# Kernel optimization log

Measured on AMD Instinct MI355X. Metric: run time of the kernel, lower is better.

## Reference

```python
import jax, jax.numpy as jnp
import numpy as np

V, E, H, T = 100000, 128, 256, 7
B, S = 64, 512
START, STOP = 5, 6
H2 = H // 2


def setup_inputs() -> dict:
    key = jax.random.key(0)
    ks = jax.random.split(key, 16)
    rn = lambda k, shape, s=0.1: jax.random.normal(k, shape, jnp.float32) * s
    inp = {}
    inp["sentence"] = jax.random.randint(ks[0], (B, S), 0, V)
    inp["tags"] = jax.random.randint(ks[1], (B, S), 0, 5)
    inp["h0"] = jax.random.normal(ks[2], (2, B, H2), jnp.float32)
    inp["c0"] = jax.random.normal(ks[3], (2, B, H2), jnp.float32)
    inp["embedding"] = rn(ks[4], (V, E), 1.0)
    inp["w_ih_f"] = rn(ks[5], (4 * H2, E)); inp["w_hh_f"] = rn(ks[6], (4 * H2, H2))
    inp["b_ih_f"] = rn(ks[7], (4 * H2,)); inp["b_hh_f"] = rn(ks[8], (4 * H2,))
    inp["w_ih_b"] = rn(ks[9], (4 * H2, E)); inp["w_hh_b"] = rn(ks[10], (4 * H2, H2))
    inp["b_ih_b"] = rn(ks[11], (4 * H2,)); inp["b_hh_b"] = rn(ks[12], (4 * H2,))
    inp["w_out"] = rn(ks[13], (T, H)); inp["b_out"] = rn(ks[14], (T,))
    trans = jax.random.normal(ks[15], (T, T), jnp.float32)
    trans = trans.at[START, :].set(-10000.0).at[:, STOP].set(-10000.0)
    inp["transitions"] = trans
    return inp


def _lstm_dir(x, h0, c0, wih, whh, bih, bhh, reverse):
    # x: [S, B, E]; PyTorch gate order i, f, g, o
    def step(carry, xt):
        h, c = carry
        z = xt @ wih.T + h @ whh.T + bih + bhh  # [B, 4*H2]
        i, f, g, o = jnp.split(z, 4, axis=-1)
        c = jax.nn.sigmoid(f) * c + jax.nn.sigmoid(i) * jnp.tanh(g)
        h = jax.nn.sigmoid(o) * jnp.tanh(c)
        return (h, c), h
    _, hs = jax.lax.scan(step, (h0, c0), x, reverse=reverse)
    return hs  # [S, B, H2]


def reference(sentence, tags, h0, c0, embedding, w_ih_f, w_hh_f, b_ih_f, b_hh_f,
              w_ih_b, w_hh_b, b_ih_b, b_hh_b, w_out, b_out, transitions):
    # Embedding; torch code does .view(S, B, -1) on a [B, S, E] tensor (raw
    # reinterpretation) -- replicate with reshape to match the math exactly.
    embeds = embedding[sentence].reshape(S, B, E)
    hf = _lstm_dir(embeds, h0[0], c0[0], w_ih_f, w_hh_f, b_ih_f, b_hh_f, False)
    hb = _lstm_dir(embeds, h0[1], c0[1], w_ih_b, w_hh_b, b_ih_b, b_hh_b, True)
    feats = jnp.concatenate([hf, hb], axis=-1) @ w_out.T + b_out  # [S, B, T]

    # CRF forward algorithm. Original uses transitions.t(), i.e. step score
    # for prev=i -> next=j is transitions[i, j].
    alpha0 = jnp.full((B, T), -10000.0, jnp.float32).at[:, START].set(0.0)
    def crf_step(alpha, feat):
        # [b, i, j]: alpha[b,i] + transitions[i,j]; LSE over i, add emit[b,j]
        a = jax.nn.logsumexp(alpha[:, :, None] + transitions[None, :, :], axis=1) + feat
        return a, None
    alpha, _ = jax.lax.scan(crf_step, alpha0, feats)
    fwd_score = jax.nn.logsumexp(alpha + transitions[STOP][None, :], axis=1)  # [B]

    # Gold path score: transitions[next, prev] + emit[next], per _score_sentence.
    tags_ext = jnp.concatenate([jnp.full((B, 1), START, tags.dtype), tags], axis=1)
    t_prev, t_next = tags_ext[:, :-1], tags_ext[:, 1:]  # [B, S]
    trans_sc = transitions[t_next, t_prev].sum(axis=1)
    emit_sc = jnp.take_along_axis(jnp.transpose(feats, (1, 0, 2)),
                                  t_next[:, :, None], axis=2)[..., 0].sum(axis=1)
    gold = trans_sc + emit_sc + transitions[STOP, tags_ext[:, -1]]
    return jnp.sum(fwd_score - gold) / B
```

## Files before the change

kernel.cpp:

```cpp
#include <hip/hip_runtime.h>

typedef unsigned int u32;
typedef unsigned short u16;
typedef __attribute__((ext_vector_type(8))) short short8;
typedef __attribute__((ext_vector_type(4))) float f32x4;

#define DEV __device__ __forceinline__
#define LOG2E 1.44269504089f

DEV u16 f2bf(float f) {
    u32 u = __float_as_uint(f);
    return (u16)((u + 0x7FFFu + ((u >> 16) & 1u)) >> 16);
}
DEV float bf2f(u16 h) { return __uint_as_float(((u32)h) << 16); }
DEV float frcp(float x) { return __builtin_amdgcn_rcpf(x); }
DEV float fexp2(float x) {
#if __has_builtin(__builtin_amdgcn_exp2f)
    return __builtin_amdgcn_exp2f(x);
#else
    return exp2f(x);
#endif
}
DEV u32 pack_bf16(float a, float b) {
#if __has_builtin(__builtin_amdgcn_cvt_pk_bf16_f32)
    auto v = __builtin_amdgcn_cvt_pk_bf16_f32(a, b);
    u32 r; __builtin_memcpy(&r, &v, 4); return r;
#else
    return (u32)f2bf(a) | ((u32)f2bf(b) << 16);
#endif
}
DEV float xex(uint2 v, int r) {
    u32 u = (r & 2) ? v.y : v.x;
    return (r & 1) ? __uint_as_float(u & 0xFFFF0000u) : __uint_as_float(u << 16);
}

__global__ __launch_bounds__(512) void k_inproj2(
    const int* __restrict__ sent, const float* __restrict__ emb,
    const float* __restrict__ wihf, const float* __restrict__ bihf, const float* __restrict__ bhhf,
    const float* __restrict__ wihb, const float* __restrict__ bihb, const float* __restrict__ bhhb,
    u16* __restrict__ Xf, u16* __restrict__ Xb)
{
    int blk = blockIdx.x;
    int d  = blk >> 7;
    int sc = blk & 127;
    const float* wih = d ? wihb : wihf;
    const float* bih = d ? bihb : bihf;
    const float* bhh = d ? bhhb : bhhf;
    u16* X = d ? Xb : Xf;
    int tid = threadIdx.x;
    int w = tid >> 6, lane = tid & 63;
    int rg = lane >> 4, cn = lane & 15;

    short8 afr[4][4];
    #pragma unroll
    for (int mi = 0; mi < 4; ++mi) {
        int gate = 16 * (w + 8 * mi) + cn;
        #pragma unroll
        for (int kt = 0; kt < 4; ++kt) {
            const float* p = wih + (size_t)gate * 128 + kt * 32 + rg * 8;
            float4 f0 = *(const float4*)p;
            float4 f1 = *(const float4*)(p + 4);
            union { short8 v; u32 u[4]; } sv;
            sv.u[0] = pack_bf16(f0.x, f0.y);
            sv.u[1] = pack_bf16(f0.z, f0.w);
            sv.u[2] = pack_bf16(f1.x, f1.y);
            sv.u[3] = pack_bf16(f1.z, f1.w);
            afr[mi][kt] = sv.v;
        }
    }
    float bs[4][4];
    #pragma unroll
    for (int mi = 0; mi < 4; ++mi)
        #pragma unroll
        for (int r = 0; r < 4; ++r) {
            int g = 16 * (w + 8 * mi) + 4 * rg + r;
            bs[mi][r] = bih[g] + bhh[g];
        }

    __shared__ u16 tile[2][64][136];
    #pragma unroll
    for (int stage = 0; stage < 2; ++stage) {
        if (stage) __syncthreads();
        {
            int row = tid >> 2, q = tid & 3;
            int sl = row >> 6, bb = row & 63;
            int tok = sent[(sc * 4 + stage * 2 + sl) * 64 + bb];
            const float* er = emb + (size_t)tok * 128 + q * 32;
            u16* dst = &tile[sl][bb][q * 32];
            #pragma unroll
            for (int u = 0; u < 4; ++u) {
                float4 a = *(const float4*)(er + u * 8);
                float4 c = *(const float4*)(er + u * 8 + 4);
                uint4 st;
                st.x = pack_bf16(a.x, a.y); st.y = pack_bf16(a.z, a.w);
                st.z = pack_bf16(c.x, c.y); st.w = pack_bf16(c.z, c.w);
                *(uint4*)(dst + u * 8) = st;
            }
        }
        __syncthreads();
        #pragma unroll
        for (int ss = 0; ss < 2; ++ss) {
            int s = sc * 4 + stage * 2 + ss;
            #pragma unroll
            for (int nt = 0; nt < 4; ++nt) {
                short8 bfr[4];
                #pragma unroll
                for (int kt = 0; kt < 4; ++kt)
                    bfr[kt] = *(const short8*)&tile[ss][nt * 16 + cn][kt * 32 + rg * 8];
                #pragma unroll
                for (int mi = 0; mi < 4; ++mi) {
                    f32x4 acc = {0.f, 0.f, 0.f, 0.f};
                    #pragma unroll
                    for (int kt = 0; kt < 4; ++kt)
                        acc = __builtin_amdgcn_mfma_f32_16x16x32_bf16(afr[mi][kt], bfr[kt], acc, 0, 0, 0);
                    size_t base = (((size_t)s * 4 + nt) * 32 + (w + 8 * mi)) * 256
                                + (size_t)rg * 64 + (size_t)cn * 4;
                    uint2 st;
                    st.x = pack_bf16((acc[0] + bs[mi][0]) * LOG2E, (acc[1] + bs[mi][1]) * LOG2E);
                    st.y = pack_bf16((acc[2] + bs[mi][2]) * LOG2E, (acc[3] + bs[mi][3]) * LOG2E);
                    *(uint2*)(X + base) = st;
                }
            }
        }
    }
}

__global__ __launch_bounds__(512) void k_lstm(
    const float* __restrict__ h0, const float* __restrict__ c0,
    const float* __restrict__ whhf, const float* __restrict__ whhb,
    const u16* __restrict__ Xf, const u16* __restrict__ Xb,
    u16* __restrict__ hfo, u16* __restrict__ hbo)
{
    int d  = blockIdx.x >> 2, g4 = blockIdx.x & 3;
    const float* whh = d ? whhb : whhf;
    const u16*   X   = d ? Xb   : Xf;
    u16*         ho  = d ? hbo  : hfo;
    int w = threadIdx.x >> 6, lane = threadIdx.x & 63;
    int rg = lane >> 4, cn = lane & 15;

    short8 afr[4][4];
    #pragma unroll
    for (int mi = 0; mi < 4; ++mi) {
        int gate = 16 * (w + 8 * mi) + cn;
        #pragma unroll
        for (int kt = 0; kt < 4; ++kt) {
            const float* p = whh + (size_t)gate * 128 + kt * 32 + rg * 8;
            float4 f0 = *(const float4*)p;
            float4 f1 = *(const float4*)(p + 4);
            union { short8 v; u32 u[4]; } sv;
            sv.u[0] = pack_bf16(f0.x * LOG2E, f0.y * LOG2E);
            sv.u[1] = pack_bf16(f0.z * LOG2E, f0.w * LOG2E);
            sv.u[2] = pack_bf16(f1.x * LOG2E, f1.y * LOG2E);
            sv.u[3] = pack_bf16(f1.z * LOG2E, f1.w * LOG2E);
            afr[mi][kt] = sv.v;
        }
    }
    int b = g4 * 16 + cn;
    int chb = 16 * w + rg * 4;
    float cst[4];
    {
        float4 cv = *(const float4*)(c0 + ((size_t)d * 64 + b) * 128 + chb);
        cst[0]=cv.x; cst[1]=cv.y; cst[2]=cv.z; cst[3]=cv.w;
    }
    __shared__ u16 hbuf[2][16][136];
    {
        float4 hv = *(const float4*)(h0 + ((size_t)d * 64 + b) * 128 + chb);
        uint2 st0;
        st0.x = pack_bf16(hv.x, hv.y);
        st0.y = pack_bf16(hv.z, hv.w);
        *(uint2*)&hbuf[0][cn][chb] = st0;
    }
    __syncthreads();

    int s0 = d ? 511 : 0;
    const int sdB = d ? -65536 : 65536;
    const int hdB = d ? -16384 : 16384;

    int voffB[4];
    #pragma unroll
    for (int mi = 0; mi < 4; ++mi)
        voffB[mi] = 2 * ((w + 8 * mi) * 256 + rg * 64 + cn * 4);
    const char* xbase = (const char*)X + ((size_t)s0 * 32768 + (size_t)g4 * 8192) * 2;
    uint2 xA[4], xB[4];
    #pragma unroll
    for (int mi = 0; mi < 4; ++mi) {
        xA[mi] = *(const uint2*)(xbase + voffB[mi]);
        xB[mi] = *(const uint2*)(xbase + sdB + voffB[mi]);
    }
    const char* sxA = xbase + 2 * sdB;
    const char* sxB = xbase + 3 * sdB;
    int vhoff = 2 * (b * 128 + chb);
    char* hsp = (char*)ho + (size_t)s0 * 16384;

#define LSTM_STEP(RB, WB, XC, SX)                                            \
    do {                                                                     \
        short8 bfr[4];                                                       \
        _Pragma("unroll")                                                    \
        for (int kt = 0; kt < 4; ++kt)                                       \
            bfr[kt] = *(const short8*)&hbuf[RB][cn][kt * 32 + rg * 8];       \
        f32x4 z[4];                                                          \
        _Pragma("unroll")                                                    \
        for (int mi = 0; mi < 4; ++mi) {                                     \
            f32x4 acc;                                                       \
            acc[0] = xex(XC[mi], 0); acc[1] = xex(XC[mi], 1);                \
            acc[2] = xex(XC[mi], 2); acc[3] = xex(XC[mi], 3);                \
            _Pragma("unroll")                                                \
            for (int kt = 0; kt < 4; ++kt)                                   \
                acc = __builtin_amdgcn_mfma_f32_16x16x32_bf16(               \
                    afr[mi][kt], bfr[kt], acc, 0, 0, 0);                     \
            z[mi] = acc;                                                     \
            XC[mi] = *(const uint2*)(SX + voffB[mi]);                        \
        }                                                                    \
        SX += 2 * sdB;                                                       \
        float hnew[4];                                                       \
        _Pragma("unroll")                                                    \
        for (int r = 0; r < 4; ++r) {                                        \
            float zi = z[0][r], zf = z[1][r], zg = z[2][r], zo = z[3][r];    \
            float ei = fexp2(-zi);                                           \
            float ef = fexp2(-zf);                                           \
            float eo = fexp2(-zo);                                           \
            float eg = fexp2(fminf(zg + zg, 126.f));                         \
            float A = 1.f + ei, F = 1.f + ef, G = 1.f + eg, O = 1.f + eo;    \
            float AG = A * G;                                                \
            float num = fmaf(cst[r], AG, (eg - 1.f) * F);                    \
            float cc  = num * frcp(F * AG);                                  \
            cst[r] = cc;                                                     \
            float ec = fexp2(fminf(2.885390082f * cc, 126.f));               \
            hnew[r] = (ec - 1.f) * frcp(fmaf(O, ec, O));                     \
        }                                                                    \
        uint2 st;                                                            \
        st.x = pack_bf16(hnew[0], hnew[1]);                                  \
        st.y = pack_bf16(hnew[2], hnew[3]);                                  \
        *(uint2*)&hbuf[WB][cn][chb] = st;                                    \
        *(uint2*)(hsp + vhoff) = st;                                         \
        hsp += hdB;                                                          \
        asm volatile("s_waitcnt lgkmcnt(0)\n\ts_barrier" ::: "memory");      \
    } while (0)

    for (int it = 0; it < 256; ++it) {
        LSTM_STEP(0, 1, xA, sxA);
        LSTM_STEP(1, 0, xB, sxB);
    }
#undef LSTM_STEP
}

__global__ __launch_bounds__(256) void k_feats(
    const u16* __restrict__ hf, const u16* __restrict__ hb,
    const float* __restrict__ wout, const float* __restrict__ bout,
    float* __restrict__ feats)
{
    __shared__ u16 sf[32][136], sb[32][136];
    __shared__ float wo[7][260];
    __shared__ float bo[8];
    int tid = threadIdx.x;
    int pos0 = blockIdx.x * 32;
    {
        int r = tid >> 3, cc = (tid & 7) * 16;
        const uint4* pf = (const uint4*)(hf + (size_t)(pos0 + r) * 128 + cc);
        const uint4* pb = (const uint4*)(hb + (size_t)(pos0 + r) * 128 + cc);
        *(uint4*)&sf[r][cc]     = pf[0];
        *(uint4*)&sf[r][cc + 8] = pf[1];
        *(uint4*)&sb[r][cc]     = pb[0];
        *(uint4*)&sb[r][cc + 8] = pb[1];
    }
    for (int i = tid; i < 1792; i += 256) wo[i >> 8][i & 255] = wout[i];
    if (tid < 7) bo[tid] = bout[tid];
    __syncthreads();
    int pp = tid >> 3, tt = tid & 7;
    if (tt < 7) {
        float acc = bo[tt];
        #pragma unroll 4
        for (int ch = 0; ch < 128; ++ch)
            acc += bf2f(sf[pp][ch]) * wo[tt][ch]
                 + bf2f(sb[pp][ch]) * wo[tt][128 + ch];
        feats[(size_t)(pos0 + pp) * 7 + tt] = acc;
    }
}

__global__ __launch_bounds__(64) void k_crf_chunk(
    const float* __restrict__ feats, const float* __restrict__ trans,
    float* __restrict__ chunkM)
{
    int b = blockIdx.x >> 3, c = blockIdx.x & 7;
    int lane = threadIdx.x;
    int i = lane >> 3, j = lane & 7;
    __shared__ float M[8][8];
    __shared__ float fl[64][8];
    int s0 = c * 64;
    for (int idx = lane; idx < 448; idx += 64) {
        int ss = idx / 7, jj = idx - ss * 7;
        fl[ss][jj] = feats[(size_t)((s0 + ss) * 64 + b) * 7 + jj];
    }
    float tc[7];
    #pragma unroll
    for (int k = 0; k < 7; ++k) tc[k] = (j < 7) ? trans[k * 7 + j] : 0.f;
    __syncthreads();
    M[i][j] = (i < 7 && j < 7) ? (trans[i * 7 + j] + fl[0][j]) : -1e30f;
    __syncthreads();
    for (int ss = 1; ss < 64; ++ss) {
        float4 m0 = *(const float4*)&M[i][0];
        float4 m1 = *(const float4*)&M[i][4];
        float v0 = m0.x + tc[0], v1 = m0.y + tc[1], v2 = m0.z + tc[2];
        float v3 = m0.w + tc[3], v4 = m1.x + tc[4], v5 = m1.y + tc[5];
        float v6 = m1.z + tc[6];
        float mx = fmaxf(fmaxf(fmaxf(v0, v1), fmaxf(v2, v3)),
                         fmaxf(fmaxf(v4, v5), v6));
        float sm = __expf(v0 - mx) + __expf(v1 - mx) + __expf(v2 - mx)
                 + __expf(v3 - mx) + __expf(v4 - mx) + __expf(v5 - mx)
                 + __expf(v6 - mx);
        float r = mx + __logf(sm) + fl[ss][j];
        __syncthreads();
        if (i < 7 && j < 7) M[i][j] = r;
        __syncthreads();
    }
    if (i < 7 && j < 7)
        chunkM[(size_t)(b * 8 + c) * 49 + i * 7 + j] = M[i][j];
}

__global__ __launch_bounds__(64) void k_crf_final(
    const float* __restrict__ chunkM, const float* __restrict__ trans,
    const int* __restrict__ tags, const float* __restrict__ feats,
    float* __restrict__ out)
{
    int b = blockIdx.x;
    int lane = threadIdx.x;
    __shared__ float P[8][49];
    __shared__ float Tl[49];
    __shared__ float av[2][8];
    __shared__ int   tg[512];
    for (int idx = lane; idx < 392; idx += 64)
        P[idx / 49][idx % 49] = chunkM[(size_t)b * 392 + idx];
    if (lane < 49) Tl[lane] = trans[lane];
    for (int idx = lane; idx < 512; idx += 64) tg[idx] = tags[(size_t)b * 512 + idx];
    if (lane < 8) av[0][lane] = (lane == 5) ? 0.f : -1e4f;
    __syncthreads();
    int cur = 0;
    for (int cch = 0; cch < 8; ++cch) {
        if (lane < 7) {
            float vv[7], mx = -1e30f;
            #pragma unroll
            for (int ii = 0; ii < 7; ++ii) {
                vv[ii] = av[cur][ii] + P[cch][ii * 7 + lane];
                mx = fmaxf(mx, vv[ii]);
            }
            float sm = 0.f;
            #pragma unroll
            for (int ii = 0; ii < 7; ++ii) sm += __expf(vv[ii] - mx);
            av[cur ^ 1][lane] = mx + __logf(sm);
        }
        __syncthreads();
        cur ^= 1;
    }
    float mx = -1e30f, uu[7];
    #pragma unroll
    for (int jj = 0; jj < 7; ++jj) {
        uu[jj] = av[cur][jj] + Tl[6 * 7 + jj];
        mx = fmaxf(mx, uu[jj]);
    }
    float sm = 0.f;
    #pragma unroll
    for (int jj = 0; jj < 7; ++jj) sm += __expf(uu[jj] - mx);
    float fwd = mx + __logf(sm);
    float acc = 0.f;
    for (int ss = lane; ss < 512; ss += 64) {
        int tn = tg[ss];
        int tp = (ss == 0) ? 5 : tg[ss - 1];
        acc += Tl[tn * 7 + tp] + feats[(size_t)(ss * 64 + b) * 7 + tn];
    }
    #pragma unroll
    for (int mk = 32; mk >= 1; mk >>= 1) acc += __shfl_xor(acc, mk, 64);
    if (lane == 0) {
        float gold = acc + Tl[6 * 7 + tg[511]];
        atomicAdd(out, (fwd - gold) * (1.0f / 64.0f));
    }
}

extern "C" void kernel_launch(void* const* d_in, const int* in_sizes, int n_in,
                              void* d_out, int out_size, void* d_ws, size_t ws_size,
                              hipStream_t stream) {
    const int*   sent = (const int*)d_in[0];
    const int*   tags = (const int*)d_in[1];
    const float* h0   = (const float*)d_in[2];
    const float* c0   = (const float*)d_in[3];
    const float* emb  = (const float*)d_in[4];
    const float* wihf = (const float*)d_in[5];
    const float* whhf = (const float*)d_in[6];
    const float* bihf = (const float*)d_in[7];
    const float* bhhf = (const float*)d_in[8];
    const float* wihb = (const float*)d_in[9];
    const float* whhb = (const float*)d_in[10];
    const float* bihb = (const float*)d_in[11];
    const float* bhhb = (const float*)d_in[12];
    const float* wout = (const float*)d_in[13];
    const float* bout = (const float*)d_in[14];
    const float* trn  = (const float*)d_in[15];

    char* ws = (char*)d_ws;
    u16*   Xf     = (u16*)(ws);
    u16*   Xb     = (u16*)(ws + 33554432);
    u16*   hfp    = (u16*)(ws + 67108864);
    u16*   hbp    = (u16*)(ws + 75497472);
    float* feats  = (float*)(ws + 83886080);
    float* chunkM = (float*)(ws + 84803584);

    hipMemsetAsync(d_out, 0, 4, stream);
    k_inproj2<<<256, 512, 0, stream>>>(sent, emb, wihf, bihf, bhhf,
                                       wihb, bihb, bhhb, Xf, Xb);
    k_lstm<<<8, 512, 0, stream>>>(h0, c0, whhf, whhb, Xf, Xb, hfp, hbp);
    k_feats<<<1024, 256, 0, stream>>>(hfp, hbp, wout, bout, feats);
    k_crf_chunk<<<512, 64, 0, stream>>>(feats, trn, chunkM);
    k_crf_final<<<64, 64, 0, stream>>>(chunkM, trn, tags, feats, (float*)d_out);
}
```

Baseline: 576.3 us.

## Fuse input projection into recurrent LSTM kernel with prefetched embedding ring

Removes the separate input-projection kernel and its 64MB bf16 intermediate. The LSTM kernel now computes the W_ih·x term each step with extra MFMAs, using embedding rows prefetched a few steps ahead into a shared ring buffer. Hidden outputs are staged in an 8-slot shared ring and written to global memory in coalesced batches every 8 steps. This doubles the MFMA work on the serial critical path in exchange for dropping global traffic and a kernel launch, and it adds an extra barrier every 8 steps.

Result: slower. 694.3 us (+20.5%).

```diff
diff --git a/kernel.cpp b/kernel.cpp
--- a/kernel.cpp
+++ b/kernel.cpp
@@ -29,192 +29,131 @@
     return (u32)f2bf(a) | ((u32)f2bf(b) << 16);
 #endif
 }
-DEV float xex(uint2 v, int r) {
-    u32 u = (r & 2) ? v.y : v.x;
-    return (r & 1) ? __uint_as_float(u & 0xFFFF0000u) : __uint_as_float(u << 16);
-}
-
-__global__ __launch_bounds__(512) void k_inproj2(
+
+__global__ __launch_bounds__(512) void k_lstm(
     const int* __restrict__ sent, const float* __restrict__ emb,
-    const float* __restrict__ wihf, const float* __restrict__ bihf, const float* __restrict__ bhhf,
-    const float* __restrict__ wihb, const float* __restrict__ bihb, const float* __restrict__ bhhb,
-    u16* __restrict__ Xf, u16* __restrict__ Xb)
+    const float* __restrict__ h0, const float* __restrict__ c0,
+    const float* __restrict__ whhf, const float* __restrict__ whhb,
+    const float* __restrict__ wihf, const float* __restrict__ wihb,
+    const float* __restrict__ bihf, const float* __restrict__ bhhf,
+    const float* __restrict__ bihb, const float* __restrict__ bhhb,
+    u16* __restrict__ hfo, u16* __restrict__ hbo)
 {
-    int blk = blockIdx.x;
-    int d  = blk >> 7;
-    int sc = blk & 127;
+    const int d  = blockIdx.x >> 2, g4 = blockIdx.x & 3;
+    const float* whh = d ? whhb : whhf;
     const float* wih = d ? wihb : wihf;
     const float* bih = d ? bihb : bihf;
     const float* bhh = d ? bhhb : bhhf;
-    u16* X = d ? Xb : Xf;
-    int tid = threadIdx.x;
-    int w = tid >> 6, lane = tid & 63;
-    int rg = lane >> 4, cn = lane & 15;
-
-    short8 afr[4][4];
+    u16* ho = d ? hbo : hfo;
+    const int tid = threadIdx.x;
+    const int w = tid >> 6, lane = tid & 63;
+    const int rg = lane >> 4, cn = lane & 15;
+    const int row16 = tid >> 5, col32 = tid & 31;
+    const int chb = 16 * w + rg * 4;
+    const int b = g4 * 16 + cn;
+
+    __shared__ int stoks[512 * 17];
+    __shared__ __align__(16) u16 ebuf[4][16][136];
+    __shared__ __align__(16) u16 hring[8][16][136];
+
+    short8 ah[4][4], ae[4][4];
     #pragma unroll
     for (int mi = 0; mi < 4; ++mi) {
         int gate = 16 * (w + 8 * mi) + cn;
         #pragma unroll
         for (int kt = 0; kt < 4; ++kt) {
-            const float* p = wih + (size_t)gate * 128 + kt * 32 + rg * 8;
-            float4 f0 = *(const float4*)p;
-            float4 f1 = *(const float4*)(p + 4);
-            union { short8 v; u32 u[4]; } sv;
-            sv.u[0] = pack_bf16(f0.x, f0.y);
-            sv.u[1] = pack_bf16(f0.z, f0.w);
-            sv.u[2] = pack_bf16(f1.x, f1.y);
-            sv.u[3] = pack_bf16(f1.z, f1.w);
-            afr[mi][kt] = sv.v;
+            const float* ph = whh + (size_t)gate * 128 + kt * 32 + rg * 8;
+            const float* pe = wih + (size_t)gate * 128 + kt * 32 + rg * 8;
+            float4 h0v = *(const float4*)ph, h1v = *(const float4*)(ph + 4);
+            float4 e0v = *(const float4*)pe, e1v = *(const float4*)(pe + 4);
+            union { short8 v; u32 u[4]; } sh, se;
+            sh.u[0] = pack_bf16(h0v.x * LOG2E, h0v.y * LOG2E);
+            sh.u[1] = pack_bf16(h0v.z * LOG2E, h0v.w * LOG2E);
+            sh.u[2] = pack_bf16(h1v.x * LOG2E, h1v.y * LOG2E);
+            sh.u[3] = pack_bf16(h1v.z * LOG2E, h1v.w * LOG2E);
+            se.u[0] = pack_bf16(e0v.x * LOG2E, e0v.y * LOG2E);
+            se.u[1] = pack_bf16(e0v.z * LOG2E, e0v.w * LOG2E);
+            se.u[2] = pack_bf16(e1v.x * LOG2E, e1v.y * LOG2E);
+            se.u[3] = pack_bf16(e1v.z * LOG2E, e1v.w * LOG2E);
+            ah[mi][kt] = sh.v;
+            ae[mi][kt] = se.v;
         }
     }
-    float bs[4][4];
+    f32x4 bs4[4];
     #pragma unroll
     for (int mi = 0; mi < 4; ++mi)
         #pragma unroll
         for (int r = 0; r < 4; ++r) {
             int g = 16 * (w + 8 * mi) + 4 * rg + r;
-            bs[mi][r] = bih[g] + bhh[g];
+            bs4[mi][r] = (bih[g] + bhh[g]) * LOG2E;
         }
-
-    __shared__ u16 tile[2][64][136];
-    #pragma unroll
-    for (int stage = 0; stage < 2; ++stage) {
-        if (stage) __syncthreads();
-        {
-            int row = tid >> 2, q = tid & 3;
-            int sl = row >> 6, bb = row & 63;
-            int tok = sent[(sc * 4 + stage * 2 + sl) * 64 + bb];
-            const float* er = emb + (size_t)tok * 128 + q * 32;
-            u16* dst = &tile[sl][bb][q * 32];
-            #pragma unroll
-            for (int u = 0; u < 4; ++u) {
-                float4 a = *(const float4*)(er + u * 8);
-                float4 c = *(const float4*)(er + u * 8 + 4);
-                uint4 st;
-                st.x = pack_bf16(a.x, a.y); st.y = pack_bf16(a.z, a.w);
-                st.z = pack_bf16(c.x, c.y); st.w = pack_bf16(c.z, c.w);
-                *(uint4*)(dst + u * 8) = st;
-            }
-        }
-        __syncthreads();
-        #pragma unroll
-        for (int ss = 0; ss < 2; ++ss) {
-            int s = sc * 4 + stage * 2 + ss;
-            #pragma unroll
-            for (int nt = 0; nt < 4; ++nt) {
-                short8 bfr[4];
-                #pragma unroll
-                for (int kt = 0; kt < 4; ++kt)
-                    bfr[kt] = *(const short8*)&tile[ss][nt * 16 + cn][kt * 32 + rg * 8];
-                #pragma unroll
-                for (int mi = 0; mi < 4; ++mi) {
-                    f32x4 acc = {0.f, 0.f, 0.f, 0.f};
-                    #pragma unroll
-                    for (int kt = 0; kt < 4; ++kt)
-                        acc = __builtin_amdgcn_mfma_f32_16x16x32_bf16(afr[mi][kt], bfr[kt], acc, 0, 0, 0);
-                    size_t base = (((size_t)s * 4 + nt) * 32 + (w + 8 * mi)) * 256
-                                + (size_t)rg * 64 + (size_t)cn * 4;
-                    uint2 st;
-                    st.x = pack_bf16((acc[0] + bs[mi][0]) * LOG2E, (acc[1] + bs[mi][1]) * LOG2E);
-                    st.y = pack_bf16((acc[2] + bs[mi][2]) * LOG2E, (acc[3] + bs[mi][3]) * LOG2E);
-                    *(uint2*)(X + base) = st;
-                }
-            }
-        }
-    }
-}
-
-__global__ __launch_bounds__(512) void k_lstm(
-    const float* __restrict__ h0, const float* __restrict__ c0,
-    const float* __restrict__ whhf, const float* __restrict__ whhb,
-    const u16* __restrict__ Xf, const u16* __restrict__ Xb,
-    u16* __restrict__ hfo, u16* __restrict__ hbo)
-{
-    int d  = blockIdx.x >> 2, g4 = blockIdx.x & 3;
-    const float* whh = d ? whhb : whhf;
-    const u16*   X   = d ? Xb   : Xf;
-    u16*         ho  = d ? hbo  : hfo;
-    int w = threadIdx.x >> 6, lane = threadIdx.x & 63;
-    int rg = lane >> 4, cn = lane & 15;
-
-    short8 afr[4][4];
-    #pragma unroll
-    for (int mi = 0; mi < 4; ++mi) {
-        int gate = 16 * (w + 8 * mi) + cn;
-        #pragma unroll
-        for (int kt = 0; kt < 4; ++kt) {
-            const float* p = whh + (size_t)gate * 128 + kt * 32 + rg * 8;
-            float4 f0 = *(const float4*)p;
-            float4 f1 = *(const float4*)(p + 4);
-            union { short8 v; u32 u[4]; } sv;
-            sv.u[0] = pack_bf16(f0.x * LOG2E, f0.y * LOG2E);
-            sv.u[1] = pack_bf16(f0.z * LOG2E, f0.w * LOG2E);
-            sv.u[2] = pack_bf16(f1.x * LOG2E, f1.y * LOG2E);
-            sv.u[3] = pack_bf16(f1.z * LOG2E, f1.w * LOG2E);
-            afr[mi][kt] = sv.v;
-        }
-    }
-    int b = g4 * 16 + cn;
-    int chb = 16 * w + rg * 4;
     float cst[4];
     {
         float4 cv = *(const float4*)(c0 + ((size_t)d * 64 + b) * 128 + chb);
         cst[0]=cv.x; cst[1]=cv.y; cst[2]=cv.z; cst[3]=cv.w;
     }
-    __shared__ u16 hbuf[2][16][136];
+    {
+        int s = tid;
+        const int4* sp = (const int4*)(sent + s * 64 + g4 * 16);
+        int4 t0 = sp[0], t1 = sp[1], t2 = sp[2], t3 = sp[3];
+        int* dst = &stoks[s * 17];
+        dst[0]=t0.x; dst[1]=t0.y; dst[2]=t0.z; dst[3]=t0.w;
+        dst[4]=t1.x; dst[5]=t1.y; dst[6]=t1.z; dst[7]=t1.w;
+        dst[8]=t2.x; dst[9]=t2.y; dst[10]=t2.z; dst[11]=t2.w;
+        dst[12]=t3.x; dst[13]=t3.y; dst[14]=t3.z; dst[15]=t3.w;
+    }
     {
         float4 hv = *(const float4*)(h0 + ((size_t)d * 64 + b) * 128 + chb);
         uint2 st0;
         st0.x = pack_bf16(hv.x, hv.y);
         st0.y = pack_bf16(hv.z, hv.w);
-        *(uint2*)&hbuf[0][cn][chb] = st0;
-    }
-    __syncthreads();
-
-    int s0 = d ? 511 : 0;
-    const int sdB = d ? -65536 : 65536;
-    const int hdB = d ? -16384 : 16384;
-
-    int voffB[4];
-    #pragma unroll
-    for (int mi = 0; mi < 4; ++mi)
-        voffB[mi] = 2 * ((w + 8 * mi) * 256 + rg * 64 + cn * 4);
-    const char* xbase = (const char*)X + ((size_t)s0 * 32768 + (size_t)g4 * 8192) * 2;
-    uint2 xA[4], xB[4];
-    #pragma unroll
-    for (int mi = 0; mi < 4; ++mi) {
-        xA[mi] = *(const uint2*)(xbase + voffB[mi]);
-        xB[mi] = *(const uint2*)(xbase + sdB + voffB[mi]);
-    }
-    const char* sxA = xbase + 2 * sdB;
-    const char* sxB = xbase + 3 * sdB;
-    int vhoff = 2 * (b * 128 + chb);
-    char* hsp = (char*)ho + (size_t)s0 * 16384;
-
-#define LSTM_STEP(RB, WB, XC, SX)                                            \
-    do {                                                                     \
-        short8 bfr[4];                                                       \
-        _Pragma("unroll")                                                    \
-        for (int kt = 0; kt < 4; ++kt)                                       \
-            bfr[kt] = *(const short8*)&hbuf[RB][cn][kt * 32 + rg * 8];       \
+        *(uint2*)&hring[7][cn][chb] = st0;
+    }
+    #pragma unroll
+    for (int k = 0; k < 2; ++k) {
+        int s = d ? (511 - k) : k;
+        int tok = sent[s * 64 + g4 * 16 + row16];
+        float4 ev = *(const float4*)(emb + (size_t)tok * 128 + col32 * 4);
+        uint2 wv; wv.x = pack_bf16(ev.x, ev.y); wv.y = pack_bf16(ev.z, ev.w);
+        *(uint2*)&ebuf[k][row16][col32 * 4] = wv;
+    }
+    float4 pA, pB;
+    { int s = d ? 509 : 2; int tok = sent[s*64 + g4*16 + row16];
+      pA = *(const float4*)(emb + (size_t)tok * 128 + col32 * 4); }
+    { int s = d ? 508 : 3; int tok = sent[s*64 + g4*16 + row16];
+      pB = *(const float4*)(emb + (size_t)tok * 128 + col32 * 4); }
+    __syncthreads();
+
+#define SUB(U, PEND)                                                         \
+    {                                                                        \
+        const int t = it * 8 + U;                                            \
+        short8 hb[4], eb[4];                                                 \
+        _Pragma("unroll") for (int kt = 0; kt < 4; ++kt) {                   \
+            hb[kt] = *(const short8*)&hring[(U + 7) & 7][cn][kt*32 + rg*8];  \
+            eb[kt] = *(const short8*)&ebuf[U & 3][cn][kt*32 + rg*8];         \
+        }                                                                    \
         f32x4 z[4];                                                          \
-        _Pragma("unroll")                                                    \
-        for (int mi = 0; mi < 4; ++mi) {                                     \
-            f32x4 acc;                                                       \
-            acc[0] = xex(XC[mi], 0); acc[1] = xex(XC[mi], 1);                \
-            acc[2] = xex(XC[mi], 2); acc[3] = xex(XC[mi], 3);                \
-            _Pragma("unroll")                                                \
-            for (int kt = 0; kt < 4; ++kt)                                   \
+        _Pragma("unroll") for (int mi = 0; mi < 4; ++mi) {                   \
+            f32x4 acc = bs4[mi];                                             \
+            _Pragma("unroll") for (int kt = 0; kt < 4; ++kt)                 \
                 acc = __builtin_amdgcn_mfma_f32_16x16x32_bf16(               \
-                    afr[mi][kt], bfr[kt], acc, 0, 0, 0);                     \
+                    ah[mi][kt], hb[kt], acc, 0, 0, 0);                       \
+            _Pragma("unroll") for (int kt = 0; kt < 4; ++kt)                 \
+                acc = __builtin_amdgcn_mfma_f32_16x16x32_bf16(               \
+                    ae[mi][kt], eb[kt], acc, 0, 0, 0);                       \
             z[mi] = acc;                                                     \
-            XC[mi] = *(const uint2*)(SX + voffB[mi]);                        \
         }                                                                    \
-        SX += 2 * sdB;                                                       \
+        {                                                                    \
+            uint2 wv; wv.x = pack_bf16(PEND.x, PEND.y);                      \
+            wv.y = pack_bf16(PEND.z, PEND.w);                                \
+            *(uint2*)&ebuf[(U + 2) & 3][row16][col32 * 4] = wv;              \
+            int s_ = d ? (511 - (t + 4)) : (t + 4);                          \
+            s_ = s_ < 0 ? 0 : (s_ > 511 ? 511 : s_);                         \
+            int tok = stoks[s_ * 17 + row16];                                \
+            PEND = *(const float4*)(emb + (size_t)tok * 128 + col32 * 4);    \
+        }                                                                    \
         float hnew[4];                                                       \
-        _Pragma("unroll")                                                    \
-        for (int r = 0; r < 4; ++r) {                                        \
+        _Pragma("unroll") for (int r = 0; r < 4; ++r) {                      \
             float zi = z[0][r], zf = z[1][r], zg = z[2][r], zo = z[3][r];    \
             float ei = fexp2(-zi);                                           \
             float ef = fexp2(-zf);                                           \
@@ -228,20 +167,27 @@
             float ec = fexp2(fminf(2.885390082f * cc, 126.f));               \
             hnew[r] = (ec - 1.f) * frcp(fmaf(O, ec, O));                     \
         }                                                                    \
-        uint2 st;                                                            \
-        st.x = pack_bf16(hnew[0], hnew[1]);                                  \
-        st.y = pack_bf16(hnew[2], hnew[3]);                                  \
-        *(uint2*)&hbuf[WB][cn][chb] = st;                                    \
-        *(uint2*)(hsp + vhoff) = st;                                         \
-        hsp += hdB;                                                          \
+        uint2 st2;                                                           \
+        st2.x = pack_bf16(hnew[0], hnew[1]);                                 \
+        st2.y = pack_bf16(hnew[2], hnew[3]);                                 \
+        *(uint2*)&hring[U & 7][cn][chb] = st2;                               \
         asm volatile("s_waitcnt lgkmcnt(0)\n\ts_barrier" ::: "memory");      \
-    } while (0)
-
-    for (int it = 0; it < 256; ++it) {
-        LSTM_STEP(0, 1, xA, sxA);
-        LSTM_STEP(1, 0, xB, sxB);
-    }
-#undef LSTM_STEP
+    }
+
+    for (int it = 0; it < 64; ++it) {
+        SUB(0, pA); SUB(1, pB); SUB(2, pA); SUB(3, pB);
+        SUB(4, pA); SUB(5, pB); SUB(6, pA); SUB(7, pB);
+        #pragma unroll
+        for (int c = 0; c < 4; ++c) {
+            int chunk = c * 512 + tid;
+            int slot = chunk >> 8, rw = (chunk >> 4) & 15, part = chunk & 15;
+            uint4 v = *(const uint4*)&hring[slot][rw][part * 8];
+            int s_ = d ? (511 - (it * 8 + slot)) : (it * 8 + slot);
+            *(uint4*)(ho + ((size_t)s_ * 64 + g4 * 16 + rw) * 128 + part * 8) = v;
+        }
+        asm volatile("s_waitcnt lgkmcnt(0)\n\ts_barrier" ::: "memory");
+    }
+#undef SUB
 }
 
 __global__ __launch_bounds__(256) void k_feats(
@@ -396,17 +342,14 @@
     const float* trn  = (const float*)d_in[15];
 
     char* ws = (char*)d_ws;
-    u16*   Xf     = (u16*)(ws);
-    u16*   Xb     = (u16*)(ws + 33554432);
-    u16*   hfp    = (u16*)(ws + 67108864);
-    u16*   hbp    = (u16*)(ws + 75497472);
-    float* feats  = (float*)(ws + 83886080);
-    float* chunkM = (float*)(ws + 84803584);
+    u16*   hfp    = (u16*)(ws);
+    u16*   hbp    = (u16*)(ws + 8388608);
+    float* feats  = (float*)(ws + 16777216);
+    float* chunkM = (float*)(ws + 17694720);
 
     hipMemsetAsync(d_out, 0, 4, stream);
-    k_inproj2<<<256, 512, 0, stream>>>(sent, emb, wihf, bihf, bhhf,
-                                       wihb, bihb, bhhb, Xf, Xb);
-    k_lstm<<<8, 512, 0, stream>>>(h0, c0, whhf, whhb, Xf, Xb, hfp, hbp);
+    k_lstm<<<8, 512, 0, stream>>>(sent, emb, h0, c0, whhf, whhb, wihf, wihb,
+                                  bihf, bhhf, bihb, bhhb, hfp, hbp);
     k_feats<<<1024, 256, 0, stream>>>(hfp, hbp, wout, bout, feats);
     k_crf_chunk<<<512, 64, 0, stream>>>(feats, trn, chunkM);
     k_crf_final<<<64, 64, 0, stream>>>(chunkM, trn, tags, feats, (float*)d_out);
```
